# Performance work log

Measured on AMD Instinct MI355X. Metric: run time of the kernel, lower is better.

Reference implementation:

```python
import jax, jax.numpy as jnp
import numpy as np

H = 64           # edge/node/global hidden size
IN_F = 4         # node_attr_size
OUT_F = 1        # out_size
NUM_EMB = 100    # edge_num_embeddings
SKIP = True


def setup_inputs() -> dict:
    key = jax.random.key(0)
    ks = jax.random.split(key, 24)
    T, N, E = 4, 20000, 320000
    NNZ = 340000
    inp = {
        'node_attr': jax.random.normal(ks[0], (T, N, IN_F), jnp.float32),
        'global_attr': jax.random.normal(ks[1], (1, H), jnp.float32),
        'L_values': jax.random.normal(ks[2], (NNZ,), jnp.float32),
        'coeff': jnp.ones((1,), jnp.float32),
        'edge_attr': jax.random.randint(ks[3], (T, E), 0, NUM_EMB),
        'edge_index': jax.random.randint(ks[4], (2, E), 0, N),
        'L_index': jax.random.randint(ks[5], (2, NNZ), 0, N),
        'num_processing_steps': 4,
        # parameters
        'emb': jax.random.normal(ks[6], (NUM_EMB, H), jnp.float32) * 0.05,
        'W_ne': jax.random.normal(ks[7], (IN_F, H), jnp.float32) * 0.1,
        'b_ne': jnp.zeros((H,), jnp.float32),
        'W_eb': jax.random.normal(ks[8], ((H + 2 * H) * 2 + H, H), jnp.float32) * 0.05,
        'b_eb': jnp.zeros((H,), jnp.float32),
        'W_nb': jax.random.normal(ks[9], (2 * H + 2 * H + H, H), jnp.float32) * 0.05,
        'b_nb': jnp.zeros((H,), jnp.float32),
        'W_gb': jax.random.normal(ks[10], (H + H + H, H), jnp.float32) * 0.05,
        'b_gb': jnp.zeros((H,), jnp.float32),
        'W_d1': jax.random.normal(ks[11], (H, H), jnp.float32) * 0.1,
        'b_d1': jnp.zeros((H,), jnp.float32),
        'W_d2': jax.random.normal(ks[12], (H, OUT_F), jnp.float32) * 0.1,
        'b_d2': jnp.zeros((OUT_F,), jnp.float32),
        'W_i1': jax.random.normal(ks[13], (H, H), jnp.float32) * 0.1,
        'b_i1': jnp.zeros((H,), jnp.float32),
        'W_i2': jax.random.normal(ks[14], (H, IN_F), jnp.float32) * 0.1,
        'b_i2': jnp.zeros((IN_F,), jnp.float32),
    }
    return inp


def reference(node_attr, global_attr, L_values, coeff, emb, W_ne, b_ne,
              W_eb, b_eb, W_nb, b_nb, W_gb, b_gb, W_d1, b_d1, W_d2, b_d2,
              W_i1, b_i1, W_i2, b_i2, edge_attr, edge_index, L_index,
              num_processing_steps):
    T, N, _ = node_attr.shape
    s, r = edge_index[0], edge_index[1]
    Li, Lj = L_index[0], L_index[1]

    # encoders (all T steps at once)
    x_enc = jax.nn.relu(node_attr @ W_ne + b_ne)   # [T,N,H]
    e_enc = emb[edge_attr]                         # [T,E,H]

    def laplacian(h):  # sparse sp_L @ h, h: [N,H]
        return jax.ops.segment_sum(L_values[:, None] * h[Lj], Li, num_segments=N)

    def step(carry, xe):
        h_x, h_e, h_g = carry
        x_t, e_t = xe
        node_cat = jnp.concatenate([x_t, h_x], axis=-1)          # [N,2H]
        edge_cat = jnp.concatenate([e_t, h_e], axis=-1)          # [E,2H]
        g = h_g[0]                                               # [H]
        E_ = edge_cat.shape[0]
        # EdgeBlock: edges + sender + receiver + globals
        eb_in = jnp.concatenate([edge_cat, node_cat[s], node_cat[r],
                                 jnp.broadcast_to(g, (E_, g.shape[0]))], axis=-1)
        e_new = jax.nn.relu(eb_in @ W_eb + b_eb)                 # [E,H]
        # NodeBlock: scatter_add aggregates of received/sent edges
        recv = jax.ops.segment_sum(e_new, r, num_segments=N)
        sent = jax.ops.segment_sum(e_new, s, num_segments=N)
        nb_in = jnp.concatenate([recv, sent, node_cat,
                                 jnp.broadcast_to(g, (N, g.shape[0]))], axis=-1)
        x_new = jax.nn.relu(nb_in @ W_nb + b_nb)                 # [N,H]
        # GlobalBlock: scatter_mean (single graph -> mean)
        gb_in = jnp.concatenate([e_new.mean(0), x_new.mean(0), g])[None]
        g_new = jax.nn.relu(gb_in @ W_gb + b_gb)                 # [1,H]
        h_x_next = h_x + x_new if SKIP else x_new
        time_d = h_x_next - h_x
        spat_d = coeff[0] * laplacian(h_x_next)  # pde='diff': coeff * L u
        return (h_x_next, e_new, g_new), (h_x_next, time_d, spat_d)

    h0 = (jnp.zeros((N, H), jnp.float32),
          jnp.zeros((e_enc.shape[1], H), jnp.float32),
          global_attr)
    _, (hid, time_d, spat_d) = jax.lax.scan(step, h0, (x_enc, e_enc))

    # decoders over all steps
    out_nodes = jax.nn.relu(hid @ W_d1 + b_d1) @ W_d2 + b_d2     # [T,N,OUT_F]
    pred_in = jax.nn.relu(hid @ W_i1 + b_i1) @ W_i2 + b_i2       # [T,N,IN_F]
    return out_nodes, time_d, spat_d, pred_in
```

## Files before the change

kernel.cpp:

```cpp
#include <hip/hip_runtime.h>

#define TT 4
#define NN 20000
#define EE 320000
#define NZ 340000
#define NBKT 2500
#define SCB 2048

typedef __attribute__((ext_vector_type(8))) __bf16 bf16x8;
typedef __attribute__((ext_vector_type(16))) float f32x16;

__device__ __forceinline__ unsigned short f2bf(float f) {
    unsigned int u = __float_as_uint(f);
    u = (u + 0x7FFFu + ((u >> 16) & 1u)) >> 16;
    return (unsigned short)u;
}
__device__ __forceinline__ float bf2f(unsigned short h) {
    return __uint_as_float(((unsigned int)h) << 16);
}

#define GLL16(src, dst) __builtin_amdgcn_global_load_lds( \
    (const __attribute__((address_space(1))) unsigned int*)(src), \
    (__attribute__((address_space(3))) unsigned int*)(dst), 16, 0, 0)

#define XB (TT * NN / 4)
#define CB ((NZ + 255) / 256)

__global__ __launch_bounds__(256) void k_setup(
    const float* __restrict__ na, const float* __restrict__ W_ne,
    const float* __restrict__ b_ne, unsigned short* __restrict__ xenc,
    const int* __restrict__ r, const int* __restrict__ s,
    const int* __restrict__ Li, int* cnt_r, int* cnt_s, int* cnt_L,
    const float* __restrict__ W_eb, const float* __restrict__ W_nb,
    const float* __restrict__ W_d1, const float* __restrict__ W_i1,
    const float* __restrict__ emb, unsigned short* __restrict__ Bpe,
    unsigned short* __restrict__ Bpu, unsigned short* __restrict__ Bpn,
    unsigned short* __restrict__ Bpd, unsigned short* __restrict__ emb_bf) {
    int bid = blockIdx.x;
    if (bid < CB) {
        int i = bid * 256 + threadIdx.x;
        if (i < EE) { atomicAdd(&cnt_r[r[i]], 1); atomicAdd(&cnt_s[s[i]], 1); }
        if (i < NZ) { atomicAdd(&cnt_L[Li[i]], 1); }
        return;
    }
    bid -= CB;
    if (bid < 96) {
        int t = bid * 256 + threadIdx.x;
        if (t < 2 * 8 * 512) {
            int i = t & 7, l = (t >> 3) & 63, kb = (t >> 9) & 7, ch = t >> 12;
            int colv = ch * 32 + (l & 31);
            int k = kb * 16 + (l >> 5) * 8 + i;
            Bpe[t] = f2bf(W_eb[k * 64 + colv]);
        }
        if (t < 4 * 8 * 512) {
            int i = t & 7, l = (t >> 3) & 63, kb = (t >> 9) & 7, g = t >> 12;
            int colv = (g & 1) * 32 + (l & 31);
            int k = 128 + (g >> 1) * 128 + kb * 16 + (l >> 5) * 8 + i;
            Bpu[t] = f2bf(W_eb[k * 64 + colv]);
        }
        if (t < 2 * 16 * 512) {
            int i = t & 7, l = (t >> 3) & 63, kb = (t >> 9) % 16, ch = t / (16 * 512);
            int colv = ch * 32 + (l & 31);
            int k = kb * 16 + (l >> 5) * 8 + i;
            Bpn[t] = f2bf(W_nb[k * 64 + colv]);
        }
        if (t < 4 * 4 * 512) {
            int i = t & 7, l = (t >> 3) & 63, kb = (t >> 9) & 3, sec = t >> 11;
            int colv = (sec & 1) * 32 + (l & 31);
            int k = kb * 16 + (l >> 5) * 8 + i;
            const float* W = (sec < 2) ? W_d1 : W_i1;
            Bpd[t] = f2bf(W[k * 64 + colv]);
        }
        if (t < 100 * 64) emb_bf[t] = f2bf(emb[t]);
        return;
    }
    bid -= 96;
    int row = bid * 4 + (threadIdx.x >> 6);
    int j = threadIdx.x & 63;
    float4 a = *(const float4*)&na[(size_t)row * 4];
    float v = b_ne[j] + a.x * W_ne[j] + a.y * W_ne[64 + j] + a.z * W_ne[128 + j] + a.w * W_ne[192 + j];
    xenc[(size_t)row * 64 + j] = f2bf(fmaxf(v, 0.f));
}

__global__ __launch_bounds__(64) void k_usr(
    int do_update, int nusr,
    const unsigned short* __restrict__ xenc_t, const unsigned short* __restrict__ hx_bf,
    const unsigned short* __restrict__ Bpu, unsigned int* __restrict__ usr,
    const float* __restrict__ W_gb, const float* __restrict__ b_gb,
    const float* __restrict__ W_eb, const float* __restrict__ b_eb,
    const float* __restrict__ W_nb, const float* __restrict__ b_nb,
    float* __restrict__ g_cur, float* __restrict__ e_sum, float* __restrict__ x_sum,
    float* __restrict__ gb_eb, float* __restrict__ gb_nb,
    int* __restrict__ cnt, int* __restrict__ rowp, int* __restrict__ wp) {
    const int ln = threadIdx.x;

    if ((int)blockIdx.x >= nusr) {
        int which = blockIdx.x - nusr;
        int* c = cnt + which * NN;
        int* row = rowp + which * (NN + 1);
        int* w = wp + which * NN;
        const int CHS = (NN + 63) / 64;
        int base = ln * CHS;
        int msum = 0;
        for (int i = 0; i < CHS; ++i) { int idx = base + i; msum += (idx < NN) ? c[idx] : 0; }
        int inc = msum;
        for (int o = 1; o < 64; o <<= 1) {
            int v = __shfl_up(inc, o, 64);
            if (ln >= o) inc += v;
        }
        int run = inc - msum;
        for (int i = 0; i < CHS; ++i) {
            int idx = base + i;
            if (idx < NN) { row[idx] = run; w[idx] = run; run += c[idx]; }
        }
        if (ln == 63) row[NN] = inc;
        return;
    }

    const int er = ln & 31, hi = ln >> 5;

    if (blockIdx.x == 0) {
        int j = ln;
        float gv = g_cur[j];
        if (do_update) {
            float a = b_gb[j];
            for (int k = 0; k < 64; ++k) a += (e_sum[k] / (float)EE) * W_gb[k * 64 + j];
            for (int k = 0; k < 64; ++k) a += (x_sum[k] / (float)NN) * W_gb[(64 + k) * 64 + j];
            for (int k = 0; k < 64; ++k) a += g_cur[k] * W_gb[(128 + k) * 64 + j];
            gv = fmaxf(a, 0.f);
            g_cur[j] = gv;
            e_sum[j] = 0.f;
            x_sum[j] = 0.f;
        }
        float a1 = b_eb[j], a2 = b_nb[j];
        for (int k = 0; k < 64; ++k) {
            float gk = __shfl(gv, k, 64);
            a1 = fmaf(gk, W_eb[(384 + k) * 64 + j], a1);
            a2 = fmaf(gk, W_nb[(256 + k) * 64 + j], a2);
        }
        gb_eb[j] = a1;
        gb_nb[j] = a2;
    }

    const int n0 = blockIdx.x * 32;
    const int n = n0 + er;

    f32x16 a0, a1, a2, a3;
    #pragma unroll
    for (int i = 0; i < 16; ++i) { a0[i] = 0.f; a1[i] = 0.f; a2[i] = 0.f; a3[i] = 0.f; }

    const unsigned short* sx = xenc_t + (size_t)64 * n + hi * 8;
    const unsigned short* sh = hx_bf + (size_t)64 * n + hi * 8;
    #pragma unroll
    for (int c = 0; c < 2; ++c) {
        const unsigned short* src = c ? sh : sx;
        #pragma unroll
        for (int kb = 0; kb < 4; ++kb) {
            bf16x8 a = *(const bf16x8*)(src + kb * 16);
            int kg = c * 4 + kb;
            bf16x8 b0 = *(const bf16x8*)&Bpu[(size_t)((0 * 8 + kg) * 64 + ln) * 8];
            bf16x8 b1 = *(const bf16x8*)&Bpu[(size_t)((1 * 8 + kg) * 64 + ln) * 8];
            bf16x8 b2 = *(const bf16x8*)&Bpu[(size_t)((2 * 8 + kg) * 64 + ln) * 8];
            bf16x8 b3 = *(const bf16x8*)&Bpu[(size_t)((3 * 8 + kg) * 64 + ln) * 8];
            a0 = __builtin_amdgcn_mfma_f32_32x32x16_bf16(a, b0, a0, 0, 0, 0);
            a1 = __builtin_amdgcn_mfma_f32_32x32x16_bf16(a, b1, a1, 0, 0, 0);
            a2 = __builtin_amdgcn_mfma_f32_32x32x16_bf16(a, b2, a2, 0, 0, 0);
            a3 = __builtin_amdgcn_mfma_f32_32x32x16_bf16(a, b3, a3, 0, 0, 0);
        }
    }
    #pragma unroll
    for (int r = 0; r < 16; ++r) {
        int row = (r & 3) + 8 * (r >> 2) + 4 * hi;
        size_t o = (size_t)(n0 + row) * 64;
        usr[o + er]      = (unsigned int)f2bf(a0[r]) | ((unsigned int)f2bf(a1[r]) << 16);
        usr[o + 32 + er] = (unsigned int)f2bf(a2[r]) | ((unsigned int)f2bf(a3[r]) << 16);
    }
}

__global__ __launch_bounds__(512) void k_edge(
    int first, int scatterb, unsigned short* __restrict__ h_e,
    const unsigned short* __restrict__ emb_bf,
    const unsigned int* __restrict__ usr, const int* __restrict__ eattr_t,
    const int* __restrict__ sidx, const int* __restrict__ ridx,
    const unsigned short* __restrict__ Bp, const float* __restrict__ gbias,
    float* __restrict__ e_sum,
    const int* __restrict__ Li, const int* __restrict__ Lj,
    const float* __restrict__ Lv,
    int* wp_r, int* wp_s, int* wp_L,
    int* col_r, int* col_s, uint2* col_L8) {
    __shared__ unsigned short sBe[8192];
    __shared__ float sRed[8][64];
    const int tid = threadIdx.x;

    if ((int)blockIdx.x < scatterb) {
        const int sbid = blockIdx.x;
        const int bucket = sbid & 7;
        const int nlo = bucket * NBKT;
        const int cid = sbid >> 3;
        const int stride = (scatterb >> 3) * 512;
        for (int i = cid * 512 + tid; i < EE; i += stride) {
            int rv = ridx[i];
            if ((unsigned)(rv - nlo) < (unsigned)NBKT)
                col_r[atomicAdd(&wp_r[rv], 1)] = i;
            int sv = sidx[i];
            if ((unsigned)(sv - nlo) < (unsigned)NBKT)
                col_s[atomicAdd(&wp_s[sv], 1)] = i;
        }
        for (int i = cid * 512 + tid; i < NZ; i += stride) {
            int lv = Li[i];
            if ((unsigned)(lv - nlo) < (unsigned)NBKT) {
                int pos = atomicAdd(&wp_L[lv], 1);
                uint2 v;
                v.x = (unsigned int)Lj[i];
                v.y = __float_as_uint(Lv[i]);
                col_L8[pos] = v;
            }
        }
        return;
    }

    const int w = tid >> 6, ln = tid & 63;
    const int er = ln & 31, hi = ln >> 5;
    const int ebase = ((int)blockIdx.x - scatterb) * 256 + w * 32;
    const int e = ebase + er;

    const int siv = sidx[ebase + er];
    const int riv = ridx[ebase + er];
    const int ai = eattr_t[e];

    #pragma unroll
    for (int i = 0; i < 2; ++i) {
        int off = i * 4096 + w * 512;
        GLL16(Bp + off + ln * 8, sBe + off);
    }

    const unsigned short* s0 = emb_bf + (size_t)64 * ai + hi * 8;
    const unsigned short* s1 = h_e + (size_t)64 * e + hi * 8;
    bf16x8 a0 = *(const bf16x8*)(s0);
    bf16x8 a1 = *(const bf16x8*)(s0 + 16);
    bf16x8 a2 = *(const bf16x8*)(s0 + 32);
    bf16x8 a3 = *(const bf16x8*)(s0 + 48);
    bf16x8 a4{}, a5{}, a6{}, a7{};
    if (!first) {
        a4 = *(const bf16x8*)(s1);
        a5 = *(const bf16x8*)(s1 + 16);
        a6 = *(const bf16x8*)(s1 + 32);
        a7 = *(const bf16x8*)(s1 + 48);
    }

    f32x16 acc0, acc1;
    #pragma unroll
    for (int i = 0; i < 16; ++i) { acc0[i] = 0.f; acc1[i] = 0.f; }

    __syncthreads();

    #define EMM(AF, KG)                                                              \
        {                                                                            \
            bf16x8 b0 = *(const bf16x8*)&sBe[(((KG)) * 64 + ln) * 8];                \
            bf16x8 b1 = *(const bf16x8*)&sBe[((8 + (KG)) * 64 + ln) * 8];            \
            acc0 = __builtin_amdgcn_mfma_f32_32x32x16_bf16(AF, b0, acc0, 0, 0, 0);   \
            acc1 = __builtin_amdgcn_mfma_f32_32x32x16_bf16(AF, b1, acc1, 0, 0, 0);   \
        }
    EMM(a0, 0) EMM(a1, 1) EMM(a2, 2) EMM(a3, 3)
    if (!first) {
        EMM(a4, 4) EMM(a5, 5) EMM(a6, 6) EMM(a7, 7)
    }
    #undef EMM

    const float gb0 = gbias[er], gb1 = gbias[er + 32];
    float cs0 = 0.f, cs1 = 0.f;
    #pragma unroll
    for (int r = 0; r < 16; ++r) {
        int row = (r & 3) + 8 * (r >> 2) + 4 * hi;
        int si_row = __shfl(siv, row, 64);
        int ri_row = __shfl(riv, row, 64);
        unsigned int us = usr[(size_t)si_row * 64 + er];
        unsigned int ur = usr[(size_t)ri_row * 64 + 32 + er];
        size_t o = (size_t)(ebase + row) * 64;
        float v0 = fmaxf(acc0[r] + bf2f((unsigned short)(us & 0xFFFF))
                                 + bf2f((unsigned short)(ur & 0xFFFF)) + gb0, 0.f);
        float v1 = fmaxf(acc1[r] + bf2f((unsigned short)(us >> 16))
                                 + bf2f((unsigned short)(ur >> 16)) + gb1, 0.f);
        cs0 += v0; cs1 += v1;
        h_e[o + er] = f2bf(v0);
        h_e[o + er + 32] = f2bf(v1);
    }
    cs0 += __shfl_xor(cs0, 32, 64);
    cs1 += __shfl_xor(cs1, 32, 64);
    if (hi == 0) { sRed[w][er] = cs0; sRed[w][er + 32] = cs1; }
    __syncthreads();
    if (w == 0) {
        float t = 0.f;
        #pragma unroll
        for (int q = 0; q < 8; ++q) t += sRed[q][ln];
        atomicAdd(&e_sum[ln], t);
    }
}

__global__ __launch_bounds__(256) void k_glap(
    int gatherb,
    const unsigned short* __restrict__ h_e, const int* __restrict__ row_r,
    const int* __restrict__ col_r, const int* __restrict__ row_s,
    const int* __restrict__ col_s, unsigned short* __restrict__ recv,
    unsigned short* __restrict__ sentb,
    const unsigned short* __restrict__ hx_bf, const int* __restrict__ row_L,
    const uint2* __restrict__ col_L8, const float* __restrict__ coeff,
    float* __restrict__ spat_prev) {
    if ((int)blockIdx.x < gatherb) {
        int t = blockIdx.x * 256 + threadIdx.x;
        int sub = t & 31, n = t >> 5;
        int g = sub & 15, which = sub >> 4;
        const int* rowp = which ? row_s : row_r;
        const int* colp = which ? col_s : col_r;
        unsigned short* outp = which ? sentb : recv;

        float a0 = 0.f, a1 = 0.f, a2 = 0.f, a3 = 0.f;
        int b0 = rowp[n], b1 = rowp[n + 1];
        for (int p = b0; p < b1; ++p) {
            uint2 v = *(const uint2*)&h_e[(size_t)64 * colp[p] + g * 4];
            a0 += bf2f((unsigned short)(v.x & 0xFFFF));
            a1 += bf2f((unsigned short)(v.x >> 16));
            a2 += bf2f((unsigned short)(v.y & 0xFFFF));
            a3 += bf2f((unsigned short)(v.y >> 16));
        }
        uint2 packed;
        packed.x = (unsigned int)f2bf(a0) | ((unsigned int)f2bf(a1) << 16);
        packed.y = (unsigned int)f2bf(a2) | ((unsigned int)f2bf(a3) << 16);
        *(uint2*)&outp[(size_t)64 * n + g * 4] = packed;
        return;
    }
    int t = ((int)blockIdx.x - gatherb) * 256 + threadIdx.x;
    int sub = t & 31, n = t >> 5;
    int g = sub & 15, half = sub >> 4;
    float a0 = 0.f, a1 = 0.f, a2 = 0.f, a3 = 0.f;
    int b0 = row_L[n], b1 = row_L[n + 1];
    int mid = b0 + ((b1 - b0) >> 1);
    int p0 = half ? mid : b0;
    int p1 = half ? b1 : mid;
    for (int p = p0; p < p1; ++p) {
        uint2 e = col_L8[p];
        float lv = __uint_as_float(e.y);
        uint2 hv = *(const uint2*)&hx_bf[(size_t)64 * e.x + g * 4];
        a0 = fmaf(lv, bf2f((unsigned short)(hv.x & 0xFFFF)), a0);
        a1 = fmaf(lv, bf2f((unsigned short)(hv.x >> 16)), a1);
        a2 = fmaf(lv, bf2f((unsigned short)(hv.y & 0xFFFF)), a2);
        a3 = fmaf(lv, bf2f((unsigned short)(hv.y >> 16)), a3);
    }
    a0 += __shfl_xor(a0, 16, 64);
    a1 += __shfl_xor(a1, 16, 64);
    a2 += __shfl_xor(a2, 16, 64);
    a3 += __shfl_xor(a3, 16, 64);
    if (half == 0) {
        float c = coeff[0];
        float4 outv = {c * a0, c * a1, c * a2, c * a3};
        *(float4*)&spat_prev[(size_t)64 * n + g * 4] = outv;
    }
}

#define NODE_CHUNK(CIDX, BASE)                                                          \
    {                                                                                   \
        const unsigned short* src = (BASE) + hi * 8;                                    \
        _Pragma("unroll") for (int kb = 0; kb < 4; ++kb) {                              \
            bf16x8 a = *(const bf16x8*)(src + kb * 16);                                 \
            bf16x8 b0 = *(const bf16x8*)&Bp[(size_t)(((CIDX)*4 + kb) * 64 + ln) * 8];   \
            bf16x8 b1 = *(const bf16x8*)&Bp[(size_t)((16 + (CIDX)*4 + kb) * 64 + ln) * 8]; \
            acc0 = __builtin_amdgcn_mfma_f32_32x32x16_bf16(a, b0, acc0, 0, 0, 0);       \
            acc1 = __builtin_amdgcn_mfma_f32_32x32x16_bf16(a, b1, acc1, 0, 0, 0);       \
        }                                                                               \
    }

__global__ __launch_bounds__(64) void k_node(
    const unsigned short* __restrict__ recv, const unsigned short* __restrict__ sentb,
    const unsigned short* __restrict__ xenc_t, float* __restrict__ h_x,
    unsigned short* __restrict__ hx_bf, const unsigned short* __restrict__ Bp,
    const float* __restrict__ gbias, float* __restrict__ x_sum,
    unsigned short* __restrict__ hid_t, float* __restrict__ timed_t) {
    const int ln = threadIdx.x;
    const int er = ln & 31, hi = ln >> 5;
    const int n0 = blockIdx.x * 32;
    const int n = n0 + er;

    f32x16 acc0, acc1;
    #pragma unroll
    for (int i = 0; i < 16; ++i) { acc0[i] = 0.f; acc1[i] = 0.f; }

    NODE_CHUNK(0, recv + (size_t)64 * n)
    NODE_CHUNK(1, sentb + (size_t)64 * n)
    NODE_CHUNK(2, xenc_t + (size_t)64 * n)
    NODE_CHUNK(3, hx_bf + (size_t)64 * n)

    const float gb0 = gbias[er], gb1 = gbias[er + 32];
    float cs0 = 0.f, cs1 = 0.f;
    #pragma unroll
    for (int r = 0; r < 16; ++r) {
        int row = (r & 3) + 8 * (r >> 2) + 4 * hi;
        size_t o = (size_t)(n0 + row) * 64;
        float x0 = fmaxf(acc0[r] + gb0, 0.f);
        float x1 = fmaxf(acc1[r] + gb1, 0.f);
        cs0 += x0; cs1 += x1;
        float hx0 = h_x[o + er] + x0;
        float hx1 = h_x[o + er + 32] + x1;
        unsigned short hb0 = f2bf(hx0), hb1 = f2bf(hx1);
        h_x[o + er] = hx0;        h_x[o + er + 32] = hx1;
        hx_bf[o + er] = hb0;      hx_bf[o + er + 32] = hb1;
        hid_t[o + er] = hb0;      hid_t[o + er + 32] = hb1;
        timed_t[o + er] = x0;     timed_t[o + er + 32] = x1;
    }
    cs0 += __shfl_xor(cs0, 32, 64);
    cs1 += __shfl_xor(cs1, 32, 64);
    if (hi == 0) {
        atomicAdd(&x_sum[er], cs0);
        atomicAdd(&x_sum[er + 32], cs1);
    }
}

__global__ __launch_bounds__(256) void k_dec(
    const unsigned short* __restrict__ hid_bf, const unsigned short* __restrict__ Bpd,
    const float* __restrict__ b_d1, const float* __restrict__ W_d2,
    const float* __restrict__ b_d2, const float* __restrict__ b_i1,
    const float* __restrict__ W_i2, const float* __restrict__ b_i2,
    float* __restrict__ out_nodes, float* __restrict__ pred_in) {
    __shared__ unsigned short sDec[4][32 * 138];
    const int tid = threadIdx.x;
    const int w = tid >> 6, ln = tid & 63;
    const int er = ln & 31, hi = ln >> 5;
    const int row0 = (blockIdx.x * 4 + w) * 32;

    f32x16 ad0, ad1, ai0, ai1;
    #pragma unroll
    for (int i = 0; i < 16; ++i) { ad0[i] = 0.f; ad1[i] = 0.f; ai0[i] = 0.f; ai1[i] = 0.f; }

    const unsigned short* src = hid_bf + (size_t)(row0 + er) * 64 + hi * 8;
    #pragma unroll
    for (int kb = 0; kb < 4; ++kb) {
        bf16x8 a = *(const bf16x8*)(src + kb * 16);
        bf16x8 bd0 = *(const bf16x8*)&Bpd[((0 * 4 + kb) * 64 + ln) * 8];
        bf16x8 bd1 = *(const bf16x8*)&Bpd[((4 + kb) * 64 + ln) * 8];
        bf16x8 bi0 = *(const bf16x8*)&Bpd[((8 + kb) * 64 + ln) * 8];
        bf16x8 bi1 = *(const bf16x8*)&Bpd[((12 + kb) * 64 + ln) * 8];
        ad0 = __builtin_amdgcn_mfma_f32_32x32x16_bf16(a, bd0, ad0, 0, 0, 0);
        ad1 = __builtin_amdgcn_mfma_f32_32x32x16_bf16(a, bd1, ad1, 0, 0, 0);
        ai0 = __builtin_amdgcn_mfma_f32_32x32x16_bf16(a, bi0, ai0, 0, 0, 0);
        ai1 = __builtin_amdgcn_mfma_f32_32x32x16_bf16(a, bi1, ai1, 0, 0, 0);
    }

    const float bd0v = b_d1[er], bd1v = b_d1[er + 32];
    const float bi0v = b_i1[er], bi1v = b_i1[er + 32];
    unsigned short* sw = &sDec[w][0];
    #pragma unroll
    for (int r = 0; r < 16; ++r) {
        int row = (r & 3) + 8 * (r >> 2) + 4 * hi;
        sw[row * 138 + er]       = f2bf(fmaxf(ad0[r] + bd0v, 0.f));
        sw[row * 138 + er + 32]  = f2bf(fmaxf(ad1[r] + bd1v, 0.f));
        sw[row * 138 + er + 64]  = f2bf(fmaxf(ai0[r] + bi0v, 0.f));
        sw[row * 138 + er + 96]  = f2bf(fmaxf(ai1[r] + bi1v, 0.f));
    }
    __syncthreads();

    const int g_row = row0 + er;
    if (hi == 0) {
        float s = 0.f;
        for (int k = 0; k < 32; ++k) {
            unsigned int u = *(const unsigned int*)&sw[er * 138 + 2 * k];
            s = fmaf(bf2f((unsigned short)(u & 0xFFFF)), W_d2[2 * k], s);
            s = fmaf(bf2f((unsigned short)(u >> 16)), W_d2[2 * k + 1], s);
        }
        out_nodes[g_row] = s + b_d2[0];
    } else {
        float s0 = 0.f, s1 = 0.f, s2 = 0.f, s3 = 0.f;
        for (int k = 0; k < 32; ++k) {
            unsigned int u = *(const unsigned int*)&sw[er * 138 + 64 + 2 * k];
            float vlo = bf2f((unsigned short)(u & 0xFFFF));
            float vhi = bf2f((unsigned short)(u >> 16));
            float4 w0 = *(const float4*)&W_i2[(2 * k) * 4];
            float4 w1 = *(const float4*)&W_i2[(2 * k + 1) * 4];
            s0 = fmaf(vlo, w0.x, fmaf(vhi, w1.x, s0));
            s1 = fmaf(vlo, w0.y, fmaf(vhi, w1.y, s1));
            s2 = fmaf(vlo, w0.z, fmaf(vhi, w1.z, s2));
            s3 = fmaf(vlo, w0.w, fmaf(vhi, w1.w, s3));
        }
        float4 pv = {s0 + b_i2[0], s1 + b_i2[1], s2 + b_i2[2], s3 + b_i2[3]};
        *(float4*)&pred_in[(size_t)4 * g_row] = pv;
    }
}

extern "C" void kernel_launch(void* const* d_in, const int* in_sizes, int n_in,
                              void* d_out, int out_size, void* d_ws, size_t ws_size,
                              hipStream_t stream) {
    (void)in_sizes; (void)n_in; (void)out_size; (void)ws_size;
    const float* node_attr   = (const float*)d_in[0];
    const float* global_attr = (const float*)d_in[1];
    const float* L_values    = (const float*)d_in[2];
    const float* coeff       = (const float*)d_in[3];
    const int*   edge_attr   = (const int*)d_in[4];
    const int*   edge_index  = (const int*)d_in[5];
    const int*   L_index     = (const int*)d_in[6];
    const float* emb  = (const float*)d_in[8];
    const float* W_ne = (const float*)d_in[9];
    const float* b_ne = (const float*)d_in[10];
    const float* W_eb = (const float*)d_in[11];
    const float* b_eb = (const float*)d_in[12];
    const float* W_nb = (const float*)d_in[13];
    const float* b_nb = (const float*)d_in[14];
    const float* W_gb = (const float*)d_in[15];
    const float* b_gb = (const float*)d_in[16];
    const float* W_d1 = (const float*)d_in[17];
    const float* b_d1 = (const float*)d_in[18];
    const float* W_d2 = (const float*)d_in[19];
    const float* b_d2 = (const float*)d_in[20];
    const float* W_i1 = (const float*)d_in[21];
    const float* b_i1 = (const float*)d_in[22];
    const float* W_i2 = (const float*)d_in[23];
    const float* b_i2 = (const float*)d_in[24];

    const int* s_idx = edge_index;
    const int* r_idx = edge_index + EE;
    const int* Li = L_index;
    const int* Lj = L_index + NZ;

    char* ws = (char*)d_ws;
    size_t off = 0;
    auto alloc = [&](size_t bytes) -> void* {
        void* p = ws + off;
        off = (off + bytes + 255) & ~(size_t)255;
        return p;
    };
    unsigned short* xenc   = (unsigned short*)alloc((size_t)TT * NN * 64 * 2);
    unsigned short* hid    = (unsigned short*)alloc((size_t)TT * NN * 64 * 2);
    float*          h_x    = (float*)alloc((size_t)NN * 64 * 4);
    unsigned short* hx_bf  = (unsigned short*)alloc((size_t)NN * 64 * 2);
    unsigned short* h_e    = (unsigned short*)alloc((size_t)EE * 64 * 2);
    unsigned short* recv   = (unsigned short*)alloc((size_t)NN * 64 * 2);
    unsigned short* sentb  = (unsigned short*)alloc((size_t)NN * 64 * 2);
    unsigned int*   usr    = (unsigned int*)alloc((size_t)NN * 64 * 4);
    float* smalls          = (float*)alloc(2048);
    unsigned short* Bpe    = (unsigned short*)alloc((size_t)2 * 8 * 512 * 2);
    unsigned short* Bpu    = (unsigned short*)alloc((size_t)4 * 8 * 512 * 2);
    unsigned short* Bpn    = (unsigned short*)alloc((size_t)2 * 16 * 512 * 2);
    unsigned short* Bpd    = (unsigned short*)alloc((size_t)4 * 4 * 512 * 2);
    unsigned short* emb_bf = (unsigned short*)alloc((size_t)100 * 64 * 2);
    int* cnt    = (int*)alloc((size_t)3 * NN * 4);
    int* rowp   = (int*)alloc((size_t)3 * (NN + 1) * 4);
    int* wp     = (int*)alloc((size_t)3 * NN * 4);
    int* col_r  = (int*)alloc((size_t)EE * 4);
    int* col_s  = (int*)alloc((size_t)EE * 4);
    uint2* col_L8 = (uint2*)alloc((size_t)NZ * 8);

    float* g_cur = smalls;
    float* e_sum = smalls + 64;
    float* x_sum = smalls + 128;
    float* gb_eb = smalls + 192;
    float* gb_nb = smalls + 256;
    int* cnt_r = cnt, *cnt_s = cnt + NN, *cnt_L = cnt + 2 * NN;
    int* row_r = rowp, *row_s = rowp + (NN + 1), *row_L = rowp + 2 * (NN + 1);
    int* wp_r = wp, *wp_s = wp + NN, *wp_L = wp + 2 * NN;

    float* out_nodes = (float*)d_out;
    float* time_d = out_nodes + (size_t)TT * NN;
    float* spat_d = time_d + (size_t)TT * NN * 64;
    float* pred_in = spat_d + (size_t)TT * NN * 64;

    hipMemsetAsync(h_x, 0, (size_t)NN * 64 * 4, stream);
    hipMemsetAsync(hx_bf, 0, (size_t)NN * 64 * 2, stream);
    hipMemsetAsync(smalls, 0, 2048, stream);
    hipMemsetAsync(cnt, 0, (size_t)3 * NN * 4, stream);
    hipMemcpyAsync(g_cur, global_attr, 64 * 4, hipMemcpyDeviceToDevice, stream);

    k_setup<<<CB + 96 + XB, 256, 0, stream>>>(node_attr, W_ne, b_ne, xenc,
                                              r_idx, s_idx, Li, cnt_r, cnt_s, cnt_L,
                                              W_eb, W_nb, W_d1, W_i1, emb,
                                              Bpe, Bpu, Bpn, Bpd, emb_bf);

    const int NUSR = NN / 32;
    const int GB = NN * 32 / 256;
    for (int t = 0; t < TT; ++t) {
        const unsigned short* xenc_t = xenc + (size_t)t * NN * 64;
        k_usr<<<NUSR + ((t == 0) ? 3 : 0), 64, 0, stream>>>(
            t > 0, NUSR, xenc_t, hx_bf, Bpu, usr,
            W_gb, b_gb, W_eb, b_eb, W_nb, b_nb,
            g_cur, e_sum, x_sum, gb_eb, gb_nb, cnt, rowp, wp);
        int scb = (t == 0) ? SCB : 0;
        k_edge<<<scb + EE / 256, 512, 0, stream>>>(
            t == 0, scb, h_e, emb_bf, usr,
            edge_attr + (size_t)t * EE, s_idx, r_idx, Bpe, gb_eb, e_sum,
            Li, Lj, L_values, wp_r, wp_s, wp_L, col_r, col_s, col_L8);
        int grid = GB + ((t > 0) ? GB : 0);
        float* spat_prev = spat_d + (size_t)((t > 0) ? t - 1 : 0) * NN * 64;
        k_glap<<<grid, 256, 0, stream>>>(GB, h_e, row_r, col_r, row_s, col_s,
                                         recv, sentb, hx_bf, row_L, col_L8, coeff,
                                         spat_prev);
        k_node<<<NN / 32, 64, 0, stream>>>(recv, sentb, xenc_t, h_x, hx_bf,
                                           Bpn, gb_nb, x_sum,
                                           hid + (size_t)t * NN * 64,
                                           time_d + (size_t)t * NN * 64);
    }
    k_glap<<<GB, 256, 0, stream>>>(0, h_e, row_r, col_r, row_s, col_s,
                                   recv, sentb, hx_bf, row_L, col_L8, coeff,
                                   spat_d + (size_t)(TT - 1) * NN * 64);
    k_dec<<<TT * NN / 128, 256, 0, stream>>>(hid, Bpd, b_d1, W_d2, b_d2,
                                             b_i1, W_i2, b_i2, out_nodes, pred_in);
}
```

Before: 660.6 us.

## Fuse next-step sender/receiver projection into node kernel via LDS h_x tile

The per-node projection of the next step's encoded features and the new h_x (the 'usr' GEMM) now runs at the end of k_node, reading h_x from a swizzled LDS tile instead of relaunching k_usr and rereading hx_bf from global memory. The global-bias update moves to a tiny single-block kernel, and the CSR prefix scan moves to a separate 1024-thread kernel. This removes one large launch per step and a global reread of h_x. In exchange k_node gains extra MFMA work, register pressure and LDS use, and adds one small serial launch per step.

```diff
diff --git a/kernel.cpp b/kernel.cpp
--- a/kernel.cpp
+++ b/kernel.cpp
@@ -82,56 +82,70 @@
     xenc[(size_t)row * 64 + j] = f2bf(fmaxf(v, 0.f));
 }
 
-__global__ __launch_bounds__(64) void k_usr(
-    int do_update, int nusr,
-    const unsigned short* __restrict__ xenc_t, const unsigned short* __restrict__ hx_bf,
-    const unsigned short* __restrict__ Bpu, unsigned int* __restrict__ usr,
+__global__ __launch_bounds__(1024) void k_scan(int* cnt, int* rowp, int* wp) {
+    int which = blockIdx.x;
+    int* c = cnt + which * NN;
+    int* row = rowp + which * (NN + 1);
+    int* w = wp + which * NN;
+    __shared__ int ssum[1024];
+    int tid = threadIdx.x;
+    const int CH = (NN + 1023) / 1024;
+    int base = tid * CH;
+    int s = 0;
+    for (int i = 0; i < CH; ++i) { int idx = base + i; s += (idx < NN) ? c[idx] : 0; }
+    ssum[tid] = s;
+    __syncthreads();
+    for (int o = 1; o < 1024; o <<= 1) {
+        int v = (tid >= o) ? ssum[tid - o] : 0;
+        __syncthreads();
+        ssum[tid] += v;
+        __syncthreads();
+    }
+    int run = (tid > 0) ? ssum[tid - 1] : 0;
+    for (int i = 0; i < CH; ++i) {
+        int idx = base + i;
+        if (idx < NN) { row[idx] = run; w[idx] = run; run += c[idx]; }
+    }
+    if (tid == 1023) row[NN] = ssum[1023];
+}
+
+__global__ __launch_bounds__(64) void k_gbias(
     const float* __restrict__ W_gb, const float* __restrict__ b_gb,
     const float* __restrict__ W_eb, const float* __restrict__ b_eb,
     const float* __restrict__ W_nb, const float* __restrict__ b_nb,
     float* __restrict__ g_cur, float* __restrict__ e_sum, float* __restrict__ x_sum,
-    float* __restrict__ gb_eb, float* __restrict__ gb_nb,
-    int* __restrict__ cnt, int* __restrict__ rowp, int* __restrict__ wp) {
+    float* __restrict__ gb_eb, float* __restrict__ gb_nb) {
+    int j = threadIdx.x;
+    float a = b_gb[j];
+    for (int k = 0; k < 64; ++k) a += (e_sum[k] / (float)EE) * W_gb[k * 64 + j];
+    for (int k = 0; k < 64; ++k) a += (x_sum[k] / (float)NN) * W_gb[(64 + k) * 64 + j];
+    for (int k = 0; k < 64; ++k) a += g_cur[k] * W_gb[(128 + k) * 64 + j];
+    float gv = fmaxf(a, 0.f);
+    g_cur[j] = gv;
+    e_sum[j] = 0.f;
+    x_sum[j] = 0.f;
+    float a1 = b_eb[j], a2 = b_nb[j];
+    for (int k = 0; k < 64; ++k) {
+        float gk = __shfl(gv, k, 64);
+        a1 = fmaf(gk, W_eb[(384 + k) * 64 + j], a1);
+        a2 = fmaf(gk, W_nb[(256 + k) * 64 + j], a2);
+    }
+    gb_eb[j] = a1;
+    gb_nb[j] = a2;
+}
+
+__global__ __launch_bounds__(64) void k_usr(
+    const unsigned short* __restrict__ xenc_t, const unsigned short* __restrict__ hx_bf,
+    const unsigned short* __restrict__ Bpu, unsigned int* __restrict__ usr,
+    const float* __restrict__ W_eb, const float* __restrict__ b_eb,
+    const float* __restrict__ W_nb, const float* __restrict__ b_nb,
+    float* __restrict__ g_cur, float* __restrict__ gb_eb, float* __restrict__ gb_nb) {
     const int ln = threadIdx.x;
-
-    if ((int)blockIdx.x >= nusr) {
-        int which = blockIdx.x - nusr;
-        int* c = cnt + which * NN;
-        int* row = rowp + which * (NN + 1);
-        int* w = wp + which * NN;
-        const int CHS = (NN + 63) / 64;
-        int base = ln * CHS;
-        int msum = 0;
-        for (int i = 0; i < CHS; ++i) { int idx = base + i; msum += (idx < NN) ? c[idx] : 0; }
-        int inc = msum;
-        for (int o = 1; o < 64; o <<= 1) {
-            int v = __shfl_up(inc, o, 64);
-            if (ln >= o) inc += v;
-        }
-        int run = inc - msum;
-        for (int i = 0; i < CHS; ++i) {
-            int idx = base + i;
-            if (idx < NN) { row[idx] = run; w[idx] = run; run += c[idx]; }
-        }
-        if (ln == 63) row[NN] = inc;
-        return;
-    }
-
     const int er = ln & 31, hi = ln >> 5;
 
     if (blockIdx.x == 0) {
         int j = ln;
         float gv = g_cur[j];
-        if (do_update) {
-            float a = b_gb[j];
-            for (int k = 0; k < 64; ++k) a += (e_sum[k] / (float)EE) * W_gb[k * 64 + j];
-            for (int k = 0; k < 64; ++k) a += (x_sum[k] / (float)NN) * W_gb[(64 + k) * 64 + j];
-            for (int k = 0; k < 64; ++k) a += g_cur[k] * W_gb[(128 + k) * 64 + j];
-            gv = fmaxf(a, 0.f);
-            g_cur[j] = gv;
-            e_sum[j] = 0.f;
-            x_sum[j] = 0.f;
-        }
         float a1 = b_eb[j], a2 = b_nb[j];
         for (int k = 0; k < 64; ++k) {
             float gk = __shfl(gv, k, 64);
@@ -370,11 +384,15 @@
     }
 
 __global__ __launch_bounds__(64) void k_node(
+    int has_next,
     const unsigned short* __restrict__ recv, const unsigned short* __restrict__ sentb,
     const unsigned short* __restrict__ xenc_t, float* __restrict__ h_x,
     unsigned short* __restrict__ hx_bf, const unsigned short* __restrict__ Bp,
     const float* __restrict__ gbias, float* __restrict__ x_sum,
-    unsigned short* __restrict__ hid_t, float* __restrict__ timed_t) {
+    unsigned short* __restrict__ hid_t, float* __restrict__ timed_t,
+    const unsigned short* __restrict__ xenc_next,
+    const unsigned short* __restrict__ Bpu, unsigned int* __restrict__ usr) {
+    __shared__ unsigned short sHx[32 * 64];
     const int ln = threadIdx.x;
     const int er = ln & 31, hi = ln >> 5;
     const int n0 = blockIdx.x * 32;
@@ -390,6 +408,7 @@
     NODE_CHUNK(3, hx_bf + (size_t)64 * n)
 
     const float gb0 = gbias[er], gb1 = gbias[er + 32];
+    const int g0 = er >> 3, w0 = er & 7;
     float cs0 = 0.f, cs1 = 0.f;
     #pragma unroll
     for (int r = 0; r < 16; ++r) {
@@ -405,12 +424,53 @@
         hx_bf[o + er] = hb0;      hx_bf[o + er + 32] = hb1;
         hid_t[o + er] = hb0;      hid_t[o + er + 32] = hb1;
         timed_t[o + er] = x0;     timed_t[o + er + 32] = x1;
+        int rs = row & 7;
+        sHx[row * 64 + (((g0 ^ rs) << 3) | w0)] = hb0;
+        sHx[row * 64 + ((((g0 + 4) ^ rs) << 3) | w0)] = hb1;
     }
     cs0 += __shfl_xor(cs0, 32, 64);
     cs1 += __shfl_xor(cs1, 32, 64);
     if (hi == 0) {
         atomicAdd(&x_sum[er], cs0);
         atomicAdd(&x_sum[er + 32], cs1);
+    }
+    if (!has_next) return;
+
+    __syncthreads();
+
+    f32x16 a0, a1, a2, a3;
+    #pragma unroll
+    for (int i = 0; i < 16; ++i) { a0[i] = 0.f; a1[i] = 0.f; a2[i] = 0.f; a3[i] = 0.f; }
+
+    const unsigned short* sx = xenc_next + (size_t)64 * n + hi * 8;
+    #pragma unroll
+    for (int c = 0; c < 2; ++c) {
+        #pragma unroll
+        for (int kb = 0; kb < 4; ++kb) {
+            bf16x8 a;
+            if (c == 0) {
+                a = *(const bf16x8*)(sx + kb * 16);
+            } else {
+                int gi = hi + 2 * kb;
+                a = *(const bf16x8*)&sHx[er * 64 + ((gi ^ (er & 7)) << 3)];
+            }
+            int kg = c * 4 + kb;
+            bf16x8 b0 = *(const bf16x8*)&Bpu[(size_t)((0 * 8 + kg) * 64 + ln) * 8];
+            bf16x8 b1 = *(const bf16x8*)&Bpu[(size_t)((1 * 8 + kg) * 64 + ln) * 8];
+            bf16x8 b2 = *(const bf16x8*)&Bpu[(size_t)((2 * 8 + kg) * 64 + ln) * 8];
+            bf16x8 b3 = *(const bf16x8*)&Bpu[(size_t)((3 * 8 + kg) * 64 + ln) * 8];
+            a0 = __builtin_amdgcn_mfma_f32_32x32x16_bf16(a, b0, a0, 0, 0, 0);
+            a1 = __builtin_amdgcn_mfma_f32_32x32x16_bf16(a, b1, a1, 0, 0, 0);
+            a2 = __builtin_amdgcn_mfma_f32_32x32x16_bf16(a, b2, a2, 0, 0, 0);
+            a3 = __builtin_amdgcn_mfma_f32_32x32x16_bf16(a, b3, a3, 0, 0, 0);
+        }
+    }
+    #pragma unroll
+    for (int r = 0; r < 16; ++r) {
+        int row = (r & 3) + 8 * (r >> 2) + 4 * hi;
+        size_t o = (size_t)(n0 + row) * 64;
+        usr[o + er]      = (unsigned int)f2bf(a0[r]) | ((unsigned int)f2bf(a1[r]) << 16);
+        usr[o + 32 + er] = (unsigned int)f2bf(a2[r]) | ((unsigned int)f2bf(a3[r]) << 16);
     }
 }
 
@@ -570,15 +630,16 @@
                                               r_idx, s_idx, Li, cnt_r, cnt_s, cnt_L,
                                               W_eb, W_nb, W_d1, W_i1, emb,
                                               Bpe, Bpu, Bpn, Bpd, emb_bf);
-
-    const int NUSR = NN / 32;
+    k_scan<<<3, 1024, 0, stream>>>(cnt, rowp, wp);
+    k_usr<<<NN / 32, 64, 0, stream>>>(xenc, hx_bf, Bpu, usr,
+                                      W_eb, b_eb, W_nb, b_nb, g_cur, gb_eb, gb_nb);
+
     const int GB = NN * 32 / 256;
     for (int t = 0; t < TT; ++t) {
         const unsigned short* xenc_t = xenc + (size_t)t * NN * 64;
-        k_usr<<<NUSR + ((t == 0) ? 3 : 0), 64, 0, stream>>>(
-            t > 0, NUSR, xenc_t, hx_bf, Bpu, usr,
-            W_gb, b_gb, W_eb, b_eb, W_nb, b_nb,
-            g_cur, e_sum, x_sum, gb_eb, gb_nb, cnt, rowp, wp);
+        if (t > 0)
+            k_gbias<<<1, 64, 0, stream>>>(W_gb, b_gb, W_eb, b_eb, W_nb, b_nb,
+                                          g_cur, e_sum, x_sum, gb_eb, gb_nb);
         int scb = (t == 0) ? SCB : 0;
         k_edge<<<scb + EE / 256, 512, 0, stream>>>(
             t == 0, scb, h_e, emb_bf, usr,
@@ -589,10 +650,13 @@
         k_glap<<<grid, 256, 0, stream>>>(GB, h_e, row_r, col_r, row_s, col_s,
                                          recv, sentb, hx_bf, row_L, col_L8, coeff,
                                          spat_prev);
-        k_node<<<NN / 32, 64, 0, stream>>>(recv, sentb, xenc_t, h_x, hx_bf,
+        const unsigned short* xenc_next =
+            xenc + (size_t)((t < TT - 1) ? t + 1 : t) * NN * 64;
+        k_node<<<NN / 32, 64, 0, stream>>>(t < TT - 1, recv, sentb, xenc_t, h_x, hx_bf,
                                            Bpn, gb_nb, x_sum,
                                            hid + (size_t)t * NN * 64,
-                                           time_d + (size_t)t * NN * 64);
+                                           time_d + (size_t)t * NN * 64,
+                                           xenc_next, Bpu, usr);
     }
     k_glap<<<GB, 256, 0, stream>>>(0, h_e, row_r, col_r, row_s, col_s,
                                    recv, sentb, hx_bf, row_L, col_L8, coeff,
```

New measurement: 631.4 us. -4.4%, faster.
